# Performance work log

Measured on AMD Instinct MI355X. Metric: run time of the kernel, lower is better.

Reference implementation:

```python
import jax, jax.numpy as jnp
import numpy as np

HIDDEN = 512
FEAT = 128   # input features to GRU (inputs last dim = FEAT + 1 shock column)
BATCH = 128
SEQ = 512
DENSE1 = 64
BN_EPS = 1e-3  # Keras BatchNormalization default epsilon


def setup_inputs() -> dict:
    key = jax.random.key(0)
    ks = jax.random.split(key, 12)
    s = 0.05
    inputs = jax.random.normal(ks[0], (BATCH, SEQ, FEAT + 1), dtype=jnp.float32)
    return {
        "inputs": inputs,
        # GRU params (Keras reset_after=True layout: gates ordered z, r, h)
        "kernel": jax.random.normal(ks[1], (FEAT, 3 * HIDDEN), jnp.float32) * s,
        "recurrent_kernel": jax.random.normal(ks[2], (HIDDEN, 3 * HIDDEN), jnp.float32) * s,
        "bias": jax.random.normal(ks[3], (2, 3 * HIDDEN), jnp.float32) * s,  # [input_bias, recurrent_bias]
        # head
        "W1": jax.random.normal(ks[4], (HIDDEN, DENSE1), jnp.float32) * s,
        "b1": jnp.zeros((DENSE1,), jnp.float32),
        "gamma": jnp.ones((DENSE1,), jnp.float32),
        "beta": jnp.zeros((DENSE1,), jnp.float32),
        "moving_mean": jnp.zeros((DENSE1,), jnp.float32),
        "moving_var": jnp.ones((DENSE1,), jnp.float32),
        "W2": jax.random.normal(ks[5], (DENSE1, 1), jnp.float32) * s,
        "b2": jnp.zeros((1,), jnp.float32),
        "W_shock": jax.random.normal(ks[6], (1,), jnp.float32),
    }


def _gru_scan(x, h0, kernel, recurrent_kernel, bias):
    # x: [B,T,F] -> scan over time. Keras GRU v2 (reset_after=True):
    #   z = sig(x Wz + bzi + h Uz + bzr); r = sig(x Wr + ...);
    #   hh = tanh(x Wh + bhi + r*(h Uh + bhr)); h = z*h + (1-z)*hh
    b_i, b_r = bias[0], bias[1]
    xt = jnp.transpose(x, (1, 0, 2))  # [T,B,F]
    # precompute input projections for all steps: [T,B,3H]
    x_proj = jnp.einsum("tbf,fh->tbh", xt, kernel) + b_i
    H = h0.shape[-1]

    def step(h, xp):
        hp = h @ recurrent_kernel + b_r  # [B,3H]
        xz, xr, xh = xp[:, :H], xp[:, H:2 * H], xp[:, 2 * H:]
        hz, hr, hh_ = hp[:, :H], hp[:, H:2 * H], hp[:, 2 * H:]
        z = jax.nn.sigmoid(xz + hz)
        r = jax.nn.sigmoid(xr + hr)
        hh = jnp.tanh(xh + r * hh_)
        h_new = z * h + (1.0 - z) * hh
        return h_new, h_new

    state, seq = jax.lax.scan(step, h0, x_proj)
    return jnp.transpose(seq, (1, 0, 2)), state  # gru_out [B,T,H], state [B,H]


def reference(inputs, kernel, recurrent_kernel, bias, W1, b1, gamma, beta,
              moving_mean, moving_var, W2, b2, W_shock):
    x = inputs[:, :, :-1]            # [B,T,F]
    shock = inputs[:, :, -1]         # [B,T]
    h0 = jnp.zeros((x.shape[0], HIDDEN), x.dtype)
    gru_out, state = _gru_scan(x, h0, kernel, recurrent_kernel, bias)
    # shock effect: tile shock to [B,T,H], * W_shock, mean over time -> [B,H]
    shock_mean = jnp.mean(shock, axis=1, keepdims=True)  # [B,1]
    state = state + shock_mean * W_shock  # broadcasts to [B,H]
    # head (inference mode: dropout is identity, BN uses moving stats)
    h = jax.nn.relu(state @ W1 + b1)
    h = (h - moving_mean) * jax.lax.rsqrt(moving_var + BN_EPS) * gamma + beta
    return h @ W2 + b2  # [B,1]
```

## Files before the change

kernel.cpp:

```cpp
#include <hip/hip_runtime.h>
#include <hip/hip_fp16.h>

typedef _Float16 f16;
typedef _Float16 f16x8 __attribute__((ext_vector_type(8)));
typedef float    f32x4 __attribute__((ext_vector_type(4)));

#define HID 512
#define FEA 128
#define ROWSTR 129
#define SEQL 512
#define DEN1 64
#define NG 8
#define WPG 32
#define MB 16
#define GC 16
#define THREADS 256
#define KTOT 640

#define WS_CTR    0
#define WS_HRING  32768
#define WS_SM     (WS_HRING + 262144)
#define WS_HPART  (WS_SM + 1024)
#define WS_END    (WS_HPART + 16384)

#define AT_LD(p)      __hip_atomic_load((p),  __ATOMIC_RELAXED, __HIP_MEMORY_SCOPE_AGENT)
#define AT_ST(p, v)   __hip_atomic_store((p), (v), __ATOMIC_RELAXED, __HIP_MEMORY_SCOPE_AGENT)

union HQ { unsigned long long u[2]; f16x8 v; };
union H4 { unsigned long long u; f16 h[4]; };

__device__ __forceinline__ float sigmoid_f(float x) {
    x = fminf(fmaxf(x, -30.f), 30.f);
    return 1.f / (1.f + __expf(-x));
}
__device__ __forceinline__ float tanh_f(float x) {
    x = fminf(fmaxf(x, -15.f), 15.f);
    float e = __expf(2.f * x);
    return (e - 1.f) / (e + 1.f);
}

__global__ __launch_bounds__(THREADS)
void gru_fused(const float* __restrict__ inp, const float* __restrict__ Wk,
               const float* __restrict__ Rk,  const float* __restrict__ bias,
               const float* __restrict__ W1,  const float* __restrict__ b1,
               const float* __restrict__ gam, const float* __restrict__ bet,
               const float* __restrict__ mmn, const float* __restrict__ mvr,
               const float* __restrict__ W2,  const float* __restrict__ b2p,
               const float* __restrict__ Wsh, float* __restrict__ out,
               char* __restrict__ ws)
{
    __shared__ __align__(16) f16 Bl[KTOT * 48];
    __shared__ float red[4096];
    __shared__ __align__(8) f16 htile[256];

    const int tid  = threadIdx.x;
    const int g    = blockIdx.x & (NG - 1);
    const int wgk  = blockIdx.x >> 3;
    const int lane = tid & 63;
    const int wave = tid >> 6;
    const int j0   = wgk * GC;

    unsigned* ctr   = (unsigned*)(ws + WS_CTR);
    f16*      hring = (f16*)(ws + WS_HRING);
    float*    smw   = (float*)(ws + WS_SM);
    float*    hpart = (float*)(ws + WS_HPART);

    for (int idx = tid; idx < KTOT * 48; idx += THREADS) {
        int kk  = idx / 48;
        int c   = idx - kk * 48;
        int col = (c >> 4) * HID + j0 + (c & 15);
        float v = (kk < HID) ? Rk[(size_t)kk * 1536 + col]
                             : Wk[(size_t)(kk - HID) * 1536 + col];
        Bl[((size_t)(kk >> 3) * 48 + c) * 8 + (kk & 7)] = (f16)v;
    }

    if (wgk < MB) {
        int b = g * MB + wgk;
        float a = 0.f;
        for (int t = tid; t < SEQL; t += THREADS)
            a += inp[((size_t)b * SEQL + t) * ROWSTR + FEA];
        red[tid] = a;
        __syncthreads();
        for (int s = THREADS / 2; s > 0; s >>= 1) {
            if (tid < s) red[tid] += red[tid + s];
            __syncthreads();
        }
        if (tid == 0) smw[b] = red[0] * (1.f / SEQL);
    }

    const int brow = tid >> 4;
    const int jcol = j0 + (tid & 15);
    const float bZ  = bias[jcol]           + bias[1536 + jcol];
    const float bR  = bias[512 + jcol]     + bias[1536 + 512 + jcol];
    const float bXH = bias[1024 + jcol];
    const float bHH = bias[1536 + 1024 + jcol];

    const int arow  = lane & 15;
    const int ahalf = lane >> 4;

    float xa[4][8];
    if (wave == 3) {
        const float* xb = inp + ((size_t)(g * MB + arow) * SEQL + 0) * ROWSTR + ahalf * 8;
        #pragma unroll
        for (int s = 0; s < 4; ++s)
            #pragma unroll
            for (int q = 0; q < 8; ++q)
                xa[s][q] = xb[s * 32 + q];
    }

    float hold = 0.f;
    __syncthreads();

    for (int t = 0; t < SEQL; ++t) {
        const int cur = t & 1;
        const unsigned long long* hq = (const unsigned long long*)
            (hring + ((size_t)cur * NG + g) * MB * HID + (size_t)arow * HID);

        f32x4 aZ = {0,0,0,0}, aR = {0,0,0,0}, aH = {0,0,0,0}, aX = {0,0,0,0};

        if (wave < 3) {
            f16x8 af[5];
            #pragma unroll
            for (int s = 0; s < 5; ++s) {
                int ks = wave * 5 + s;
                HQ x;
                x.u[0] = AT_LD(hq + ks * 8 + ahalf * 2);
                x.u[1] = AT_LD(hq + ks * 8 + ahalf * 2 + 1);
                af[s] = x.v;
            }
            #pragma unroll
            for (int s = 0; s < 5; ++s) {
                int ks = wave * 5 + s;
                const f16x8* bp = ((const f16x8*)Bl) + (ks * 4 + ahalf) * 48 + (lane & 15);
                f16x8 bz = bp[0], br = bp[16], bh = bp[32];
                aZ = __builtin_amdgcn_mfma_f32_16x16x32_f16(af[s], bz, aZ, 0, 0, 0);
                aR = __builtin_amdgcn_mfma_f32_16x16x32_f16(af[s], br, aR, 0, 0, 0);
                aH = __builtin_amdgcn_mfma_f32_16x16x32_f16(af[s], bh, aH, 0, 0, 0);
            }
        } else {
            HQ x0;
            x0.u[0] = AT_LD(hq + 15 * 8 + ahalf * 2);
            x0.u[1] = AT_LD(hq + 15 * 8 + ahalf * 2 + 1);
            f16x8 af0 = x0.v;
            f16x8 afx[4];
            #pragma unroll
            for (int s = 0; s < 4; ++s) {
                f16x8 a;
                #pragma unroll
                for (int q = 0; q < 8; ++q) a[q] = (f16)xa[s][q];
                afx[s] = a;
            }
            {
                int tt = (t + 1 < SEQL) ? t + 1 : SEQL - 1;
                const float* xb = inp + ((size_t)(g * MB + arow) * SEQL + tt) * ROWSTR + ahalf * 8;
                #pragma unroll
                for (int s = 0; s < 4; ++s)
                    #pragma unroll
                    for (int q = 0; q < 8; ++q)
                        xa[s][q] = xb[s * 32 + q];
            }
            {
                const f16x8* bp = ((const f16x8*)Bl) + (15 * 4 + ahalf) * 48 + (lane & 15);
                aZ = __builtin_amdgcn_mfma_f32_16x16x32_f16(af0, bp[0],  aZ, 0, 0, 0);
                aR = __builtin_amdgcn_mfma_f32_16x16x32_f16(af0, bp[16], aR, 0, 0, 0);
                aH = __builtin_amdgcn_mfma_f32_16x16x32_f16(af0, bp[32], aH, 0, 0, 0);
            }
            #pragma unroll
            for (int s = 0; s < 4; ++s) {
                int ks = 16 + s;
                const f16x8* bp = ((const f16x8*)Bl) + (ks * 4 + ahalf) * 48 + (lane & 15);
                aZ = __builtin_amdgcn_mfma_f32_16x16x32_f16(afx[s], bp[0],  aZ, 0, 0, 0);
                aR = __builtin_amdgcn_mfma_f32_16x16x32_f16(afx[s], bp[16], aR, 0, 0, 0);
                aX = __builtin_amdgcn_mfma_f32_16x16x32_f16(afx[s], bp[32], aX, 0, 0, 0);
            }
        }

        #pragma unroll
        for (int i = 0; i < 4; ++i) {
            int ridx = (ahalf * 4 + i) * 16 + (lane & 15);
            red[wave * 1024 +       ridx] = aZ[i];
            red[wave * 1024 + 256 + ridx] = aR[i];
            red[wave * 1024 + 512 + ridx] = aH[i];
        }
        if (wave == 3) {
            #pragma unroll
            for (int i = 0; i < 4; ++i) {
                int ridx = (ahalf * 4 + i) * 16 + (lane & 15);
                red[3 * 1024 + 768 + ridx] = aX[i];
            }
        }
        __syncthreads();

        float zp = red[tid] + red[1024 + tid] + red[2048 + tid] + red[3072 + tid];
        float rp = red[256 + tid] + red[1280 + tid] + red[2304 + tid] + red[3328 + tid];
        float hp = red[512 + tid] + red[1536 + tid] + red[2560 + tid] + red[3584 + tid];
        float xp = red[3840 + tid];

        float z = sigmoid_f(zp + bZ);
        float r = sigmoid_f(rp + bR);
        float hcand = tanh_f((xp + bXH) + r * (hp + bHH));
        float hnew = z * hold + (1.f - z) * hcand;
        f16 h16 = (f16)hnew;
        hold = (float)h16;
        htile[brow * 16 + (tid & 15)] = h16;
        __syncthreads();

        if (tid < 64) {
            int row = tid >> 2, q = tid & 3;
            unsigned long long val = *(const unsigned long long*)(htile + row * 16 + q * 4);
            unsigned long long* dst = (unsigned long long*)
                (hring + (((size_t)(cur ^ 1) * NG + g) * MB + row) * HID + j0 + q * 4);
            AT_ST(dst, val);
        }
        if (wave == 0) {
            asm volatile("s_waitcnt vmcnt(0)" ::: "memory");
            if (tid == 0) {
                unsigned* c9 = ctr + (size_t)t * NG + g;
                unsigned old = __hip_atomic_fetch_add(c9, 1u, __ATOMIC_RELAXED, __HIP_MEMORY_SCOPE_AGENT);
                if (old != WPG - 1)
                    while (AT_LD(c9) < WPG) {}
            }
        }
        __syncthreads();
    }

    const unsigned long long* hfq = (const unsigned long long*)
        (hring + ((size_t)g * MB + brow) * HID);
    const int sub = tid & 15;
    const int c0 = wgk * 2;
    float p0 = 0.f, p1 = 0.f, w0 = 0.f, w1 = 0.f;
    for (int c8 = 0; c8 < 8; ++c8) {
        H4 x; x.u = AT_LD(hfq + sub * 8 + c8);
        #pragma unroll
        for (int e = 0; e < 4; ++e) {
            int k = sub * 32 + c8 * 4 + e;
            float hv = (float)x.h[e];
            float a0 = W1[(size_t)k * DEN1 + c0];
            float a1 = W1[(size_t)k * DEN1 + c0 + 1];
            p0 += hv * a0; p1 += hv * a1; w0 += a0; w1 += a1;
        }
    }
    red[tid] = p0; red[256 + tid] = w0; red[512 + tid] = p1; red[768 + tid] = w1;
    __syncthreads();
    if (tid < 32) {
        int b = tid >> 1, cc = tid & 1;
        int c = c0 + cc;
        float dot = 0.f, wsum = 0.f;
        for (int i = 0; i < 16; ++i) {
            dot  += red[cc * 512 + b * 16 + i];
            wsum += red[cc * 512 + 256 + b * 16 + i];
        }
        float sW = smw[g * MB + b] * Wsh[0];
        float d = dot + sW * wsum + b1[c];
        d = fmaxf(d, 0.f);
        d = (d - mmn[c]) * rsqrtf(mvr[c] + 0.001f) * gam[c] + bet[c];
        red[1024 + tid] = d * W2[c];
    }
    __syncthreads();
    if (tid < MB)
        hpart[((size_t)g * WPG + wgk) * MB + tid] = red[1024 + tid * 2] + red[1024 + tid * 2 + 1];
    __syncthreads();
    if (tid == 0) {
        __builtin_amdgcn_fence(__ATOMIC_RELEASE, "agent");
        unsigned* c9 = ctr + (size_t)SEQL * NG + g;
        unsigned old = __hip_atomic_fetch_add(c9, 1u, __ATOMIC_RELAXED, __HIP_MEMORY_SCOPE_AGENT);
        if (old != WPG - 1)
            while (AT_LD(c9) < WPG) {}
        __builtin_amdgcn_fence(__ATOMIC_ACQUIRE, "agent");
    }
    __syncthreads();
    if (wgk == 0 && tid < MB) {
        float o = b2p[0];
        for (int k = 0; k < WPG; ++k)
            o += hpart[((size_t)g * WPG + k) * MB + tid];
        out[g * MB + tid] = o;
    }
}

extern "C" void kernel_launch(void* const* d_in, const int* in_sizes, int n_in,
                              void* d_out, int out_size, void* d_ws, size_t ws_size,
                              hipStream_t stream) {
    (void)in_sizes; (void)n_in; (void)out_size; (void)ws_size;
    const float* inp  = (const float*)d_in[0];
    const float* Wk   = (const float*)d_in[1];
    const float* Rk   = (const float*)d_in[2];
    const float* bias = (const float*)d_in[3];
    const float* W1   = (const float*)d_in[4];
    const float* b1   = (const float*)d_in[5];
    const float* gam  = (const float*)d_in[6];
    const float* bet  = (const float*)d_in[7];
    const float* mmn  = (const float*)d_in[8];
    const float* mvr  = (const float*)d_in[9];
    const float* W2   = (const float*)d_in[10];
    const float* b2p  = (const float*)d_in[11];
    const float* Wsh  = (const float*)d_in[12];

    hipMemsetAsync(d_ws, 0, WS_END, stream);
    hipLaunchKernelGGL(gru_fused, dim3(NG * WPG), dim3(THREADS), 0, stream,
                       inp, Wk, Rk, bias, W1, b1, gam, bet, mmn, mvr, W2, b2p, Wsh,
                       (float*)d_out, (char*)d_ws);
}
```

Measured before the change: 1.622 ms.

## Replace per-step atomic counter barrier with per-block flag array polled wave-wide

The per-timestep inter-block barrier changes from a shared atomic fetch_add counter to one flag slot per block. Each block writes its step number to its slot, and a whole wave polls all 32 slots with a vote, which removes contention on one atomic. Hidden-state exchange loads and stores now use inline asm with sc0 sc1 cache bypass and 16-byte loads. The next-step input prefetch also moves after the MFMA work. The workspace layout shrinks, and correct visibility now depends on the hand-written cache bits and waitcnt placement.

```diff
diff --git a/kernel.cpp b/kernel.cpp
--- a/kernel.cpp
+++ b/kernel.cpp
@@ -18,16 +18,37 @@
 #define KTOT 640
 
 #define WS_CTR    0
-#define WS_HRING  32768
+#define WS_FLG    256
+#define WS_HRING  4096
 #define WS_SM     (WS_HRING + 262144)
 #define WS_HPART  (WS_SM + 1024)
 #define WS_END    (WS_HPART + 16384)
 
-#define AT_LD(p)      __hip_atomic_load((p),  __ATOMIC_RELAXED, __HIP_MEMORY_SCOPE_AGENT)
-#define AT_ST(p, v)   __hip_atomic_store((p), (v), __ATOMIC_RELAXED, __HIP_MEMORY_SCOPE_AGENT)
-
-union HQ { unsigned long long u[2]; f16x8 v; };
+#define AT_LD(p)  __hip_atomic_load((p),  __ATOMIC_RELAXED, __HIP_MEMORY_SCOPE_AGENT)
+
 union H4 { unsigned long long u; f16 h[4]; };
+
+__device__ __forceinline__ f16x8 ld_h16(const f16* p) {
+    f16x8 r;
+    asm volatile("global_load_dwordx4 %0, %1, off sc0 sc1" : "=v"(r) : "v"(p));
+    return r;
+}
+__device__ __forceinline__ void st_h64(void* p, unsigned long long v) {
+    asm volatile("global_store_dwordx2 %0, %1, off sc0 sc1" :: "v"(p), "v"(v) : "memory");
+}
+__device__ __forceinline__ unsigned ld_flag(const unsigned* p) {
+    unsigned r;
+    asm volatile("global_load_dword %0, %1, off sc0 sc1" : "=v"(r) : "v"(p) : "memory");
+    asm volatile("s_waitcnt vmcnt(0)" ::: "memory");
+    return r;
+}
+__device__ __forceinline__ void st_flag(unsigned* p, unsigned v) {
+    asm volatile("global_store_dword %0, %1, off sc0 sc1" :: "v"(p), "v"(v) : "memory");
+}
+__device__ __forceinline__ void wait_vm0() {
+    asm volatile("s_waitcnt vmcnt(0)" ::: "memory");
+    __builtin_amdgcn_sched_barrier(0);
+}
 
 __device__ __forceinline__ float sigmoid_f(float x) {
     x = fminf(fmaxf(x, -30.f), 30.f);
@@ -61,6 +82,7 @@
     const int j0   = wgk * GC;
 
     unsigned* ctr   = (unsigned*)(ws + WS_CTR);
+    unsigned* flg   = (unsigned*)(ws + WS_FLG);
     f16*      hring = (f16*)(ws + WS_HRING);
     float*    smw   = (float*)(ws + WS_SM);
     float*    hpart = (float*)(ws + WS_HPART);
@@ -113,21 +135,17 @@
 
     for (int t = 0; t < SEQL; ++t) {
         const int cur = t & 1;
-        const unsigned long long* hq = (const unsigned long long*)
-            (hring + ((size_t)cur * NG + g) * MB * HID + (size_t)arow * HID);
+        const f16* hb = hring + ((size_t)cur * NG + g) * MB * HID
+                              + (size_t)arow * HID + ahalf * 8;
 
         f32x4 aZ = {0,0,0,0}, aR = {0,0,0,0}, aH = {0,0,0,0}, aX = {0,0,0,0};
 
         if (wave < 3) {
             f16x8 af[5];
             #pragma unroll
-            for (int s = 0; s < 5; ++s) {
-                int ks = wave * 5 + s;
-                HQ x;
-                x.u[0] = AT_LD(hq + ks * 8 + ahalf * 2);
-                x.u[1] = AT_LD(hq + ks * 8 + ahalf * 2 + 1);
-                af[s] = x.v;
-            }
+            for (int s = 0; s < 5; ++s)
+                af[s] = ld_h16(hb + (wave * 5 + s) * 32);
+            wait_vm0();
             #pragma unroll
             for (int s = 0; s < 5; ++s) {
                 int ks = wave * 5 + s;
@@ -138,10 +156,7 @@
                 aH = __builtin_amdgcn_mfma_f32_16x16x32_f16(af[s], bh, aH, 0, 0, 0);
             }
         } else {
-            HQ x0;
-            x0.u[0] = AT_LD(hq + 15 * 8 + ahalf * 2);
-            x0.u[1] = AT_LD(hq + 15 * 8 + ahalf * 2 + 1);
-            f16x8 af0 = x0.v;
+            f16x8 af0 = ld_h16(hb + 15 * 32);
             f16x8 afx[4];
             #pragma unroll
             for (int s = 0; s < 4; ++s) {
@@ -149,6 +164,36 @@
                 #pragma unroll
                 for (int q = 0; q < 8; ++q) a[q] = (f16)xa[s][q];
                 afx[s] = a;
+            }
+            wait_vm0();
+            {
+                const f16x8* bp = ((const f16x8*)Bl) + (15 * 4 + ahalf) * 48 + (lane & 15);
+                aZ = __builtin_amdgcn_mfma_f32_16x16x32_f16(af0, bp[0],  aZ, 0, 0, 0);
+                aR = __builtin_amdgcn_mfma_f32_16x16x32_f16(af0, bp[16], aR, 0, 0, 0);
+                aH = __builtin_amdgcn_mfma_f32_16x16x32_f16(af0, bp[32], aH, 0, 0, 0);
+            }
+            #pragma unroll
+            for (int s = 0; s < 4; ++s) {
+                int ks = 16 + s;
+                const f16x8* bp = ((const f16x8*)Bl) + (ks * 4 + ahalf) * 48 + (lane & 15);
+                aZ = __builtin_amdgcn_mfma_f32_16x16x32_f16(afx[s], bp[0],  aZ, 0, 0, 0);
+                aR = __builtin_amdgcn_mfma_f32_16x16x32_f16(afx[s], bp[16], aR, 0, 0, 0);
+                aX = __builtin_amdgcn_mfma_f32_16x16x32_f16(afx[s], bp[32], aX, 0, 0, 0);
+            }
+        }
+
+        #pragma unroll
+        for (int i = 0; i < 4; ++i) {
+            int ridx = (ahalf * 4 + i) * 16 + (lane & 15);
+            red[wave * 1024 +       ridx] = aZ[i];
+            red[wave * 1024 + 256 + ridx] = aR[i];
+            red[wave * 1024 + 512 + ridx] = aH[i];
+        }
+        if (wave == 3) {
+            #pragma unroll
+            for (int i = 0; i < 4; ++i) {
+                int ridx = (ahalf * 4 + i) * 16 + (lane & 15);
+                red[3 * 1024 + 768 + ridx] = aX[i];
             }
             {
                 int tt = (t + 1 < SEQL) ? t + 1 : SEQL - 1;
@@ -159,35 +204,6 @@
                     for (int q = 0; q < 8; ++q)
                         xa[s][q] = xb[s * 32 + q];
             }
-            {
-                const f16x8* bp = ((const f16x8*)Bl) + (15 * 4 + ahalf) * 48 + (lane & 15);
-                aZ = __builtin_amdgcn_mfma_f32_16x16x32_f16(af0, bp[0],  aZ, 0, 0, 0);
-                aR = __builtin_amdgcn_mfma_f32_16x16x32_f16(af0, bp[16], aR, 0, 0, 0);
-                aH = __builtin_amdgcn_mfma_f32_16x16x32_f16(af0, bp[32], aH, 0, 0, 0);
-            }
-            #pragma unroll
-            for (int s = 0; s < 4; ++s) {
-                int ks = 16 + s;
-                const f16x8* bp = ((const f16x8*)Bl) + (ks * 4 + ahalf) * 48 + (lane & 15);
-                aZ = __builtin_amdgcn_mfma_f32_16x16x32_f16(afx[s], bp[0],  aZ, 0, 0, 0);
-                aR = __builtin_amdgcn_mfma_f32_16x16x32_f16(afx[s], bp[16], aR, 0, 0, 0);
-                aX = __builtin_amdgcn_mfma_f32_16x16x32_f16(afx[s], bp[32], aX, 0, 0, 0);
-            }
-        }
-
-        #pragma unroll
-        for (int i = 0; i < 4; ++i) {
-            int ridx = (ahalf * 4 + i) * 16 + (lane & 15);
-            red[wave * 1024 +       ridx] = aZ[i];
-            red[wave * 1024 + 256 + ridx] = aR[i];
-            red[wave * 1024 + 512 + ridx] = aH[i];
-        }
-        if (wave == 3) {
-            #pragma unroll
-            for (int i = 0; i < 4; ++i) {
-                int ridx = (ahalf * 4 + i) * 16 + (lane & 15);
-                red[3 * 1024 + 768 + ridx] = aX[i];
-            }
         }
         __syncthreads();
 
@@ -208,17 +224,15 @@
         if (tid < 64) {
             int row = tid >> 2, q = tid & 3;
             unsigned long long val = *(const unsigned long long*)(htile + row * 16 + q * 4);
-            unsigned long long* dst = (unsigned long long*)
-                (hring + (((size_t)(cur ^ 1) * NG + g) * MB + row) * HID + j0 + q * 4);
-            AT_ST(dst, val);
+            st_h64(hring + (((size_t)(cur ^ 1) * NG + g) * MB + row) * HID + j0 + q * 4, val);
         }
         if (wave == 0) {
             asm volatile("s_waitcnt vmcnt(0)" ::: "memory");
-            if (tid == 0) {
-                unsigned* c9 = ctr + (size_t)t * NG + g;
-                unsigned old = __hip_atomic_fetch_add(c9, 1u, __ATOMIC_RELAXED, __HIP_MEMORY_SCOPE_AGENT);
-                if (old != WPG - 1)
-                    while (AT_LD(c9) < WPG) {}
+            if (lane == 0) st_flag(flg + g * 32 + wgk, (unsigned)(t + 1));
+            const unsigned want = (unsigned)(t + 1);
+            for (;;) {
+                unsigned v = ld_flag(flg + g * 32 + (lane & 31));
+                if (__all((int)(v >= want))) break;
             }
         }
         __syncthreads();
@@ -262,10 +276,10 @@
     __syncthreads();
     if (tid == 0) {
         __builtin_amdgcn_fence(__ATOMIC_RELEASE, "agent");
-        unsigned* c9 = ctr + (size_t)SEQL * NG + g;
+        unsigned* c9 = ctr + g;
         unsigned old = __hip_atomic_fetch_add(c9, 1u, __ATOMIC_RELAXED, __HIP_MEMORY_SCOPE_AGENT);
         if (old != WPG - 1)
-            while (AT_LD(c9) < WPG) {}
+            while (__hip_atomic_load(c9, __ATOMIC_RELAXED, __HIP_MEMORY_SCOPE_AGENT) < WPG) {}
         __builtin_amdgcn_fence(__ATOMIC_ACQUIRE, "agent");
     }
     __syncthreads();
```

Result: faster. 1.386 ms (-14.6%).
